# Optimization experiments

Measured on AMD Instinct MI355X. Metric: run time of the kernel, lower is better.

The kernel has to match this reference:

```python
import jax, jax.numpy as jnp
import numpy as np
from jax import lax

DIM = 256          # C
D_INNER = 512      # expand * dim
D_STATE = 16       # N
DT_RANK = 32       # ceil(d_inner / 16)
K_CONV = 4


def setup_inputs() -> dict:
    key = jax.random.key(0)
    ks = jax.random.split(key, 20)
    B, C, H, W = 2, DIM, 64, 64
    Di, N, R = D_INNER, D_STATE, DT_RANK
    s = 0.02
    inp = {
        "decoder_feat": jax.random.normal(ks[0], (B, C, H, W), jnp.float32),
        "encoder_feat": jax.random.normal(ks[1], (B, C, H, W), jnp.float32),
        # CrossMambaFusion params
        "dec_w": jax.random.normal(ks[2], (C, 2 * Di), jnp.float32) * s,
        "dec_b": jnp.zeros((2 * Di,), jnp.float32),
        "enc_w": jax.random.normal(ks[3], (C, Di), jnp.float32) * s,
        "enc_b": jnp.zeros((Di,), jnp.float32),
        "out_w": jax.random.normal(ks[4], (Di, C), jnp.float32) * s,
        "out_b": jnp.zeros((C,), jnp.float32),
        "ln_g": jnp.ones((C,), jnp.float32),
        "ln_b": jnp.zeros((C,), jnp.float32),
        # Mamba block params (inner dim = Di, expand=1.0)
        "in_w": jax.random.normal(ks[5], (Di, 2 * Di), jnp.float32) * s,
        "in_b": jnp.zeros((2 * Di,), jnp.float32),
        "conv_w": jax.random.normal(ks[6], (Di, 1, K_CONV), jnp.float32) * 0.1,
        "conv_b": jnp.zeros((Di,), jnp.float32),
        "x_proj_w": jax.random.normal(ks[7], (Di, R + 2 * N), jnp.float32) * s,
        "dt_w": jax.random.normal(ks[8], (R, Di), jnp.float32) * 0.1,
        "dt_b": jax.random.uniform(ks[9], (Di,), jnp.float32, -4.0, -2.0),  # small dt after softplus
        "A_log": jnp.log(jnp.tile(jnp.arange(1, N + 1, dtype=jnp.float32)[None, :], (Di, 1))),
        "D_param": jnp.ones((Di,), jnp.float32),
        "m_out_w": jax.random.normal(ks[10], (Di, Di), jnp.float32) * s,
        "m_out_b": jnp.zeros((Di,), jnp.float32),
    }
    return inp


def _mamba(x, in_w, in_b, conv_w, conv_b, x_proj_w, dt_w, dt_b, A_log, D_param, m_out_w, m_out_b):
    # x: (B, L, Di)
    Bsz, L, Di = x.shape
    N, R = D_STATE, DT_RANK
    xz = x @ in_w + in_b                      # (B, L, 2*Di)
    xm, z = jnp.split(xz, 2, axis=-1)
    # causal depthwise conv over the sequence axis
    xc = jnp.swapaxes(xm, 1, 2)               # (B, Di, L)
    xc = lax.conv_general_dilated(
        xc, conv_w, window_strides=(1,), padding=[(K_CONV - 1, 0)],
        dimension_numbers=("NCH", "OIH", "NCH"), feature_group_count=Di)
    xc = xc + conv_b[None, :, None]
    u = jax.nn.silu(jnp.swapaxes(xc, 1, 2))   # (B, L, Di)
    x_dbl = u @ x_proj_w                      # (B, L, R+2N)
    dt = jax.nn.softplus(x_dbl[..., :R] @ dt_w + dt_b)   # (B, L, Di)
    Bm = x_dbl[..., R:R + N]                  # (B, L, N)
    Cm = x_dbl[..., R + N:]                   # (B, L, N)
    A = -jnp.exp(A_log)                       # (Di, N)

    def step(h, t):
        dt_t, u_t, B_t, C_t = t               # (B,Di),(B,Di),(B,N),(B,N)
        dA = jnp.exp(dt_t[..., None] * A)     # (B, Di, N)
        h = h * dA + (dt_t * u_t)[..., None] * B_t[:, None, :]
        y = jnp.einsum("bdn,bn->bd", h, C_t)
        return h, y

    h0 = jnp.zeros((Bsz, Di, N), x.dtype)
    _, ys = lax.scan(step, h0, (jnp.swapaxes(dt, 0, 1), jnp.swapaxes(u, 0, 1),
                                jnp.swapaxes(Bm, 0, 1), jnp.swapaxes(Cm, 0, 1)))
    y = jnp.swapaxes(ys, 0, 1) + u * D_param  # skip connection via D
    y = y * jax.nn.silu(z)
    return y @ m_out_w + m_out_b


def reference(decoder_feat, encoder_feat, dec_w, dec_b, enc_w, enc_b, out_w, out_b,
              ln_g, ln_b, in_w, in_b, conv_w, conv_b, x_proj_w, dt_w, dt_b,
              A_log, D_param, m_out_w, m_out_b):
    B, C, H, W = decoder_feat.shape
    Di = D_INNER
    dec = jnp.transpose(decoder_feat, (0, 2, 3, 1)).reshape(B, H * W, C)
    enc = jnp.transpose(encoder_feat, (0, 2, 3, 1)).reshape(B, H * W, C)
    dec_proj = dec @ dec_w + dec_b
    dec_x, dec_gate = dec_proj[..., :Di], dec_proj[..., Di:]
    enc_p = enc @ enc_w + enc_b
    combined = dec_x * jax.nn.sigmoid(enc_p) + enc_p          # (B, L, Di)
    processed = _mamba(combined, in_w, in_b, conv_w, conv_b, x_proj_w,
                       dt_w, dt_b, A_log, D_param, m_out_w, m_out_b)
    out = (processed * jax.nn.sigmoid(dec_gate)) @ out_w + out_b
    res = out + dec
    mu = jnp.mean(res, axis=-1, keepdims=True)
    var = jnp.mean(jnp.square(res - mu), axis=-1, keepdims=True)
    res = (res - mu) * lax.rsqrt(var + 1e-5) * ln_g + ln_b
    return jnp.transpose(res.reshape(B, H, W, C), (0, 3, 1, 2))
```

## Files before the change

kernel.cpp:

```cpp
#include <hip/hip_runtime.h>
#include <hip/hip_bf16.h>

typedef __bf16 bf16x8_t __attribute__((ext_vector_type(8)));
typedef float f32x4_t __attribute__((ext_vector_type(4)));

__device__ __forceinline__ float sigmoidf_(float x) { return 1.0f / (1.0f + __expf(-x)); }
__device__ __forceinline__ float siluf_(float x) { return x * sigmoidf_(x); }
__device__ __forceinline__ float softplusf_(float x) {
    return fmaxf(x, 0.0f) + log1pf(__expf(-fabsf(x)));
}
__device__ __forceinline__ float b2f(ushort u) { return __uint_as_float(((unsigned)u) << 16); }

__global__ __launch_bounds__(256) void k_prep(
    const float* __restrict__ dec_w, const float* __restrict__ enc_w,
    const float* __restrict__ in_w, const float* __restrict__ m_out_w,
    const float* __restrict__ out_w, const float* __restrict__ x_proj_w,
    const float* __restrict__ dt_w,
    const float* __restrict__ dec, const float* __restrict__ enc,
    __hip_bfloat16* __restrict__ dec_wT, __hip_bfloat16* __restrict__ enc_wT,
    __hip_bfloat16* __restrict__ in_wT, __hip_bfloat16* __restrict__ m_out_wT,
    __hip_bfloat16* __restrict__ out_wT, __hip_bfloat16* __restrict__ xpwT,
    __hip_bfloat16* __restrict__ dtwT,
    __hip_bfloat16* __restrict__ decL, __hip_bfloat16* __restrict__ encL)
{
    __shared__ float tile[64][65];
    if (blockIdx.x < 5312) {
        int gid = blockIdx.x * 256 + threadIdx.x;
        const float* src; __hip_bfloat16* dst; int lk, N, idx;
        if (gid < 262144)       { src = dec_w;    dst = dec_wT;   lk = 8; N = 1024; idx = gid; }
        else if (gid < 393216)  { src = enc_w;    dst = enc_wT;   lk = 8; N = 512;  idx = gid - 262144; }
        else if (gid < 917504)  { src = in_w;     dst = in_wT;    lk = 9; N = 1024; idx = gid - 393216; }
        else if (gid < 1179648) { src = m_out_w;  dst = m_out_wT; lk = 9; N = 512;  idx = gid - 917504; }
        else if (gid < 1310720) { src = out_w;    dst = out_wT;   lk = 9; N = 256;  idx = gid - 1179648; }
        else if (gid < 1343488) { src = x_proj_w; dst = xpwT;     lk = 9; N = 64;   idx = gid - 1310720; }
        else                    { src = dt_w;     dst = dtwT;     lk = 5; N = 512;  idx = gid - 1343488; }
        int K = 1 << lk;
        int n = idx >> lk, k = idx & (K - 1);
        dst[idx] = __float2bfloat16(src[(size_t)k * N + n]);
        return;
    }
    const int bid = blockIdx.x - 5312;
    const int t = threadIdx.x;
    const int ct = bid & 3;
    const int lt = (bid >> 2) & 63;
    const int sel = bid >> 8;
    const int b = sel & 1, ten = sel >> 1;
    const float* src = ten ? enc : dec;
    __hip_bfloat16* dst = ten ? encL : decL;
    const size_t ibase = (size_t)b * 256 * 4096 + (size_t)(ct * 64) * 4096 + (size_t)lt * 64;
#pragma unroll
    for (int i = 0; i < 16; ++i) {
        int c = i * 4 + (t >> 6), l = t & 63;
        tile[c][l] = src[ibase + (size_t)c * 4096 + l];
    }
    __syncthreads();
    const size_t obase = ((size_t)b * 4096 + (size_t)lt * 64) * 256 + ct * 64;
#pragma unroll
    for (int i = 0; i < 16; ++i) {
        int l = i * 4 + (t >> 6), c = t & 63;
        dst[obase + (size_t)l * 256 + c] = __float2bfloat16(tile[c][l]);
    }
}

template <int EPI, int K>
__global__ __launch_bounds__(256) void bgemm(
    const __hip_bfloat16* __restrict__ A, const __hip_bfloat16* __restrict__ Bt,
    const float* __restrict__ bias, void* __restrict__ out0,
    void* __restrict__ out1, const void* __restrict__ extra)
{
    __shared__ ushort At[128 * 32];
    __shared__ ushort Bl[128 * 32];
    const int tid = threadIdx.x;
    const int wave = tid >> 6, lane = tid & 63;
    const int n0 = blockIdx.x * 128, m0 = blockIdx.y * 128;
    const int wm = (wave >> 1) * 64, wn = (wave & 1) * 64;
    f32x4_t acc[4][4] = {};
    const int fr = lane & 15, fq = (lane >> 4) * 8;

    for (int k0 = 0; k0 < K; k0 += 32) {
#pragma unroll
        for (int q = 0; q < 2; ++q) {
            int idx = q * 256 + tid;
            int row = idx >> 2, ch = (idx & 3) * 8;
            uint4 va = *(const uint4*)&A[(size_t)(m0 + row) * K + k0 + ch];
            uint4 vb = *(const uint4*)&Bt[(size_t)(n0 + row) * K + k0 + ch];
            *(uint4*)&At[row * 32 + ch] = va;
            *(uint4*)&Bl[row * 32 + ch] = vb;
        }
        __syncthreads();
        bf16x8_t af[4], bf[4];
#pragma unroll
        for (int i = 0; i < 4; ++i) {
            af[i] = *(bf16x8_t*)&At[(wm + i * 16 + fr) * 32 + fq];
            bf[i] = *(bf16x8_t*)&Bl[(wn + i * 16 + fr) * 32 + fq];
        }
#pragma unroll
        for (int i = 0; i < 4; ++i)
#pragma unroll
            for (int j = 0; j < 4; ++j)
                acc[i][j] = __builtin_amdgcn_mfma_f32_16x16x32_bf16(af[i], bf[j], acc[i][j], 0, 0, 0);
        __syncthreads();
    }

    const int col = lane & 15, rbase = (lane >> 4) * 4;
#pragma unroll
    for (int i = 0; i < 4; ++i) {
#pragma unroll
        for (int j = 0; j < 4; ++j) {
#pragma unroll
            for (int r = 0; r < 4; ++r) {
                int m = m0 + wm + i * 16 + rbase + r;
                int n = n0 + wn + j * 16 + col;
                float v = acc[i][j][r] + bias[n];
                if (EPI == 0) {
                    ((__hip_bfloat16*)out0)[(size_t)m * 512 + n] = __float2bfloat16(v);
                } else if (EPI == 1) {
                    if (n < 512) {
                        float ep = __bfloat162float(((const __hip_bfloat16*)extra)[(size_t)m * 512 + n]);
                        ((__hip_bfloat16*)out0)[(size_t)m * 512 + n] =
                            __float2bfloat16(fmaf(v, sigmoidf_(ep), ep));
                    } else {
                        ((__hip_bfloat16*)out1)[(size_t)m * 512 + (n - 512)] =
                            __float2bfloat16(sigmoidf_(v));
                    }
                } else if (EPI == 2) {
                    if (n < 512)
                        ((__hip_bfloat16*)out0)[(size_t)m * 512 + n] = __float2bfloat16(v);
                    else
                        ((__hip_bfloat16*)out1)[(size_t)m * 512 + (n - 512)] =
                            __float2bfloat16(siluf_(v));
                } else {
                    float g = __bfloat162float(((const __hip_bfloat16*)extra)[(size_t)m * 512 + n]);
                    ((__hip_bfloat16*)out0)[(size_t)m * 512 + n] = __float2bfloat16(v * g);
                }
            }
        }
    }
}

#define CROWS 16
__global__ __launch_bounds__(256) void k_conv_proj(
    const __hip_bfloat16* __restrict__ xm, const float* __restrict__ conv_w,
    const float* __restrict__ conv_b, const __hip_bfloat16* __restrict__ xpwT,
    const __hip_bfloat16* __restrict__ dtwT, const float* __restrict__ dt_b,
    __hip_bfloat16* __restrict__ u_out, float* __restrict__ Bm,
    float* __restrict__ Cm, float* __restrict__ dt_out)
{
    __shared__ ushort ut[CROWS][512 + 8];
    __shared__ ushort adt[CROWS][32 + 8];
    const int tid = threadIdx.x;
    const int wave = tid >> 6, lane = tid & 63;
    const int bl0 = blockIdx.x * CROWS;
    const int l0 = bl0 & 4095;
    const int fr = lane & 15, fq = (lane >> 4) * 8;
    const int col = lane & 15, rbase = (lane >> 4) * 4;

    {
        const int d0 = tid * 2;
        float cw0[4], cw1[4];
#pragma unroll
        for (int k = 0; k < 4; ++k) {
            cw0[k] = conv_w[d0 * 4 + k];
            cw1[k] = conv_w[d0 * 4 + 4 + k];
        }
        const float cb0 = conv_b[d0], cb1 = conv_b[d0 + 1];
        float xa[CROWS + 3], xb[CROWS + 3];
        const ushort* xs = (const ushort*)xm;
#pragma unroll
        for (int i = 0; i < CROWS + 3; ++i) {
            if (l0 - 3 + i >= 0) {
                ushort2 v = *(const ushort2*)&xs[(size_t)(bl0 - 3 + i) * 512 + d0];
                xa[i] = b2f(v.x); xb[i] = b2f(v.y);
            } else { xa[i] = 0.f; xb[i] = 0.f; }
        }
#pragma unroll
        for (int r = 0; r < CROWS; ++r) {
            float a = cb0, b = cb1;
#pragma unroll
            for (int k = 0; k < 4; ++k) {
                a = fmaf(cw0[k], xa[r + k], a);
                b = fmaf(cw1[k], xb[r + k], b);
            }
            float ua = siluf_(a), ub = siluf_(b);
            ushort2 up = make_ushort2(
                (ushort)(__bfloat16_as_ushort(__float2bfloat16(ua))),
                (ushort)(__bfloat16_as_ushort(__float2bfloat16(ub))));
            *(ushort2*)&ut[r][d0] = up;
            *(ushort2*)&((ushort*)u_out)[(size_t)(bl0 + r) * 512 + d0] = up;
        }
    }
    __syncthreads();

    {
        f32x4_t acc = {};
        const __hip_bfloat16* bp = xpwT + (size_t)(wave * 16 + fr) * 512;
#pragma unroll
        for (int k0 = 0; k0 < 512; k0 += 32) {
            bf16x8_t af = *(bf16x8_t*)&ut[fr][k0 + fq];
            bf16x8_t bf = *(const bf16x8_t*)&bp[k0 + fq];
            acc = __builtin_amdgcn_mfma_f32_16x16x32_bf16(af, bf, acc, 0, 0, 0);
        }
#pragma unroll
        for (int r = 0; r < 4; ++r) {
            int m = rbase + r;
            int n = wave * 16 + col;
            float v = acc[r];
            if (n < 32)      adt[m][n] = (ushort)__bfloat16_as_ushort(__float2bfloat16(v));
            else if (n < 48) Bm[(size_t)(bl0 + m) * 16 + (n - 32)] = v;
            else             Cm[(size_t)(bl0 + m) * 16 + (n - 48)] = v;
        }
    }
    __syncthreads();

    {
        bf16x8_t af = *(bf16x8_t*)&adt[fr][fq];
#pragma unroll
        for (int t = 0; t < 8; ++t) {
            int nt = wave * 8 + t;
            bf16x8_t bf = *(const bf16x8_t*)&dtwT[(size_t)(nt * 16 + fr) * 32 + fq];
            f32x4_t acc = {};
            acc = __builtin_amdgcn_mfma_f32_16x16x32_bf16(af, bf, acc, 0, 0, 0);
#pragma unroll
            for (int r = 0; r < 4; ++r) {
                int m = rbase + r;
                int n = nt * 16 + col;
                dt_out[(size_t)(bl0 + m) * 512 + n] = softplusf_(acc[r] + dt_b[n]);
            }
        }
    }
}

#define CHUNK 32
#define NCHUNK 128

__global__ __launch_bounds__(512) void k_scan_part(
    const float* __restrict__ dt, const __hip_bfloat16* __restrict__ u,
    const float* __restrict__ Bmp, const float* __restrict__ A_log,
    float* __restrict__ hpart, float* __restrict__ dtsums)
{
    __shared__ float Bs[CHUNK * 16];
    const int d = threadIdx.x;
    const int chunk = blockIdx.x & (NCHUNK - 1);
    const int b = blockIdx.x >> 7;
    const size_t row0 = (size_t)b * 4096 + (size_t)chunk * CHUNK;

    Bs[d] = Bmp[row0 * 16 + d];
    float Av[16];
#pragma unroll
    for (int n = 0; n < 16; n += 4) {
        float4 al = *(const float4*)&A_log[d * 16 + n];
        Av[n + 0] = -__expf(al.x);
        Av[n + 1] = -__expf(al.y);
        Av[n + 2] = -__expf(al.z);
        Av[n + 3] = -__expf(al.w);
    }
    __syncthreads();

    const float* dtp = dt + row0 * 512 + d;
    const __hip_bfloat16* up = u + row0 * 512 + d;
    float h[16] = {};
    float dtsum = 0.f;
    for (int t = 0; t < CHUNK; ++t) {
        float dtv = dtp[(size_t)t * 512];
        float uv = __bfloat162float(up[(size_t)t * 512]);
        float dtu = dtv * uv;
        dtsum += dtv;
        const float* Bt = &Bs[t * 16];
#pragma unroll
        for (int n = 0; n < 16; ++n)
            h[n] = fmaf(h[n], __expf(dtv * Av[n]), dtu * Bt[n]);
    }
    const size_t sidx = ((size_t)b * NCHUNK + chunk) * 512 + d;
    const size_t idx = sidx * 16;
#pragma unroll
    for (int n = 0; n < 16; n += 4)
        *(float4*)&hpart[idx + n] = make_float4(h[n], h[n + 1], h[n + 2], h[n + 3]);
    dtsums[sidx] = dtsum;
}

__global__ __launch_bounds__(256) void k_scan_comb(
    const float* __restrict__ hpart, const float* __restrict__ dtsums,
    const float* __restrict__ A_log, float* __restrict__ h_in)
{
    const int gid = blockIdx.x * 256 + threadIdx.x;
    const int n = gid & 15;
    const int d = (gid >> 4) & 511;
    const int b = gid >> 13;
    const float Av = -__expf(A_log[d * 16 + n]);
    float h = 0.f;
    for (int c = 0; c < NCHUNK; ++c) {
        const size_t sidx = ((size_t)b * NCHUNK + c) * 512 + d;
        const size_t idx = sidx * 16 + n;
        h_in[idx] = h;
        h = fmaf(h, __expf(Av * dtsums[sidx]), hpart[idx]);
    }
}

__global__ __launch_bounds__(512) void k_scan_fin(
    const float* __restrict__ dt, const __hip_bfloat16* __restrict__ u,
    const float* __restrict__ Bmp, const float* __restrict__ Cmp,
    const float* __restrict__ A_log, const float* __restrict__ Dp,
    const __hip_bfloat16* __restrict__ zs, const float* __restrict__ h_in,
    __hip_bfloat16* __restrict__ yout)
{
    __shared__ float Bs[CHUNK * 16];
    __shared__ float Cs[CHUNK * 16];
    const int d = threadIdx.x;
    const int chunk = blockIdx.x & (NCHUNK - 1);
    const int b = blockIdx.x >> 7;
    const size_t row0 = (size_t)b * 4096 + (size_t)chunk * CHUNK;

    Bs[d] = Bmp[row0 * 16 + d];
    Cs[d] = Cmp[row0 * 16 + d];
    float Av[16];
#pragma unroll
    for (int n = 0; n < 16; n += 4) {
        float4 al = *(const float4*)&A_log[d * 16 + n];
        Av[n + 0] = -__expf(al.x);
        Av[n + 1] = -__expf(al.y);
        Av[n + 2] = -__expf(al.z);
        Av[n + 3] = -__expf(al.w);
    }
    const float Dv = Dp[d];
    float h[16];
    const size_t idx = (((size_t)b * NCHUNK + chunk) * 512 + d) * 16;
#pragma unroll
    for (int n = 0; n < 16; n += 4) {
        float4 hv = *(const float4*)&h_in[idx + n];
        h[n] = hv.x; h[n + 1] = hv.y; h[n + 2] = hv.z; h[n + 3] = hv.w;
    }
    __syncthreads();

    const float* dtp = dt + row0 * 512 + d;
    const __hip_bfloat16* up = u + row0 * 512 + d;
    const __hip_bfloat16* zp = zs + row0 * 512 + d;
    __hip_bfloat16* yp = yout + row0 * 512 + d;
    for (int t = 0; t < CHUNK; ++t) {
        float dtv = dtp[(size_t)t * 512];
        float uv = __bfloat162float(up[(size_t)t * 512]);
        float zv = __bfloat162float(zp[(size_t)t * 512]);
        float dtu = dtv * uv;
        const float* Bt = &Bs[t * 16];
        const float* Ct = &Cs[t * 16];
        float y = 0.f;
#pragma unroll
        for (int n = 0; n < 16; ++n) {
            h[n] = fmaf(h[n], __expf(dtv * Av[n]), dtu * Bt[n]);
            y = fmaf(h[n], Ct[n], y);
        }
        yp[(size_t)t * 512] = __float2bfloat16((y + uv * Dv) * zv);
    }
}

__global__ __launch_bounds__(256) void k_out_ln(
    const __hip_bfloat16* __restrict__ A, const __hip_bfloat16* __restrict__ Bt,
    const float* __restrict__ bias, const __hip_bfloat16* __restrict__ decL,
    const float* __restrict__ ln_g, const float* __restrict__ ln_b,
    float* __restrict__ outp)
{
    __shared__ ushort At[64 * 32];
    __shared__ ushort Bl[256 * 32];
    __shared__ float red[4][64][2];
    __shared__ float lmu[64], lsc[64];
    const int tid = threadIdx.x;
    const int wave = tid >> 6, lane = tid & 63;
    const int m0 = blockIdx.x * 64;
    const int wn = wave * 64;
    f32x4_t acc[4][4] = {};
    const int fr = lane & 15, fq = (lane >> 4) * 8;

    for (int k0 = 0; k0 < 512; k0 += 32) {
        {
            int row = tid >> 2, ch = (tid & 3) * 8;
            *(uint4*)&At[row * 32 + ch] = *(const uint4*)&A[(size_t)(m0 + row) * 512 + k0 + ch];
        }
#pragma unroll
        for (int q = 0; q < 4; ++q) {
            int idx = q * 256 + tid;
            int row = idx >> 2, ch = (idx & 3) * 8;
            *(uint4*)&Bl[row * 32 + ch] = *(const uint4*)&Bt[(size_t)row * 512 + k0 + ch];
        }
        __syncthreads();
        bf16x8_t af[4], bf[4];
#pragma unroll
        for (int i = 0; i < 4; ++i) {
            af[i] = *(bf16x8_t*)&At[(i * 16 + fr) * 32 + fq];
            bf[i] = *(bf16x8_t*)&Bl[(wn + i * 16 + fr) * 32 + fq];
        }
#pragma unroll
        for (int i = 0; i < 4; ++i)
#pragma unroll
            for (int j = 0; j < 4; ++j)
                acc[i][j] = __builtin_amdgcn_mfma_f32_16x16x32_bf16(af[i], bf[j], acc[i][j], 0, 0, 0);
        __syncthreads();
    }

    const int col = lane & 15, rbase = (lane >> 4) * 4;
#pragma unroll
    for (int i = 0; i < 4; ++i) {
#pragma unroll
        for (int r = 0; r < 4; ++r) {
            int ml = i * 16 + rbase + r;
            int m = m0 + ml;
            float s = 0.f, sq = 0.f;
#pragma unroll
            for (int j = 0; j < 4; ++j) {
                int n = wn + j * 16 + col;
                float dv = b2f(((const ushort*)decL)[(size_t)m * 256 + n]);
                float v = acc[i][j][r] + bias[n] + dv;
                acc[i][j][r] = v;
                s += v;
                sq = fmaf(v, v, sq);
            }
            s += __shfl_xor(s, 1);  sq += __shfl_xor(sq, 1);
            s += __shfl_xor(s, 2);  sq += __shfl_xor(sq, 2);
            s += __shfl_xor(s, 4);  sq += __shfl_xor(sq, 4);
            s += __shfl_xor(s, 8);  sq += __shfl_xor(sq, 8);
            if (col == 0) { red[wave][ml][0] = s; red[wave][ml][1] = sq; }
        }
    }
    __syncthreads();
    if (tid < 64) {
        float s  = red[0][tid][0] + red[1][tid][0] + red[2][tid][0] + red[3][tid][0];
        float sq = red[0][tid][1] + red[1][tid][1] + red[2][tid][1] + red[3][tid][1];
        float mu = s * (1.0f / 256.0f);
        float var = sq * (1.0f / 256.0f) - mu * mu;
        lmu[tid] = mu;
        lsc[tid] = rsqrtf(var + 1e-5f);
    }
    __syncthreads();
    const int bb = m0 >> 12;
    const int lpos0 = m0 & 4095;
#pragma unroll
    for (int i = 0; i < 4; ++i) {
#pragma unroll
        for (int r = 0; r < 4; ++r) {
            int ml = i * 16 + rbase + r;
            float mu = lmu[ml], sc = lsc[ml];
#pragma unroll
            for (int j = 0; j < 4; ++j) {
                int n = wn + j * 16 + col;
                float v = (acc[i][j][r] - mu) * sc * ln_g[n] + ln_b[n];
                outp[(size_t)bb * (256 * 4096) + (size_t)n * 4096 + lpos0 + ml] = v;
            }
        }
    }
}

extern "C" void kernel_launch(void* const* d_in, const int* in_sizes, int n_in,
                              void* d_out, int out_size, void* d_ws, size_t ws_size,
                              hipStream_t stream)
{
    const float* decoder_feat = (const float*)d_in[0];
    const float* encoder_feat = (const float*)d_in[1];
    const float* dec_w = (const float*)d_in[2];
    const float* dec_b = (const float*)d_in[3];
    const float* enc_w = (const float*)d_in[4];
    const float* enc_b = (const float*)d_in[5];
    const float* out_w = (const float*)d_in[6];
    const float* out_b = (const float*)d_in[7];
    const float* ln_g = (const float*)d_in[8];
    const float* ln_bb = (const float*)d_in[9];
    const float* in_w = (const float*)d_in[10];
    const float* in_b = (const float*)d_in[11];
    const float* conv_w = (const float*)d_in[12];
    const float* conv_b = (const float*)d_in[13];
    const float* x_proj_w = (const float*)d_in[14];
    const float* dt_w = (const float*)d_in[15];
    const float* dt_b = (const float*)d_in[16];
    const float* A_log = (const float*)d_in[17];
    const float* D_param = (const float*)d_in[18];
    const float* m_out_w = (const float*)d_in[19];
    const float* m_out_b = (const float*)d_in[20];

    float* outp = (float*)d_out;
    char* ws = (char*)d_ws;
    const size_t MB = 1024ull * 1024;
    __hip_bfloat16* decL     = (__hip_bfloat16*)(ws + 0 * MB);
    __hip_bfloat16* encL     = (__hip_bfloat16*)(ws + 4 * MB);
    __hip_bfloat16* dec_wT   = (__hip_bfloat16*)(ws + 8 * MB);
    __hip_bfloat16* enc_wT   = (__hip_bfloat16*)(ws + 9 * MB);
    __hip_bfloat16* in_wT    = (__hip_bfloat16*)(ws + 10 * MB);
    __hip_bfloat16* m_out_wT = (__hip_bfloat16*)(ws + 11 * MB);
    __hip_bfloat16* out_wT   = (__hip_bfloat16*)(ws + 12 * MB);
    __hip_bfloat16* xpwT     = (__hip_bfloat16*)(ws + 12 * MB + 262144);
    __hip_bfloat16* dtwT     = (__hip_bfloat16*)(ws + 12 * MB + 262144 + 65536);
    __hip_bfloat16* enc_pb   = (__hip_bfloat16*)(ws + 13 * MB);
    __hip_bfloat16* combined = (__hip_bfloat16*)(ws + 29 * MB);
    __hip_bfloat16* gate_sig = (__hip_bfloat16*)(ws + 37 * MB);
    __hip_bfloat16* xm       = (__hip_bfloat16*)(ws + 53 * MB);
    __hip_bfloat16* z_silu   = (__hip_bfloat16*)(ws + 61 * MB);
    __hip_bfloat16* u_buf    = (__hip_bfloat16*)(ws + 69 * MB);
    float* dt_buf            = (float*)(ws + 77 * MB);
    float* Bm                = (float*)(ws + 93 * MB);
    float* Cm                = (float*)(ws + 93 * MB + 524288);
    float* hpart  = (float*)(ws + 13 * MB);
    float* dtsums = (float*)(ws + 21 * MB);
    float* h_in   = (float*)xm;
    __hip_bfloat16* y_buf = combined;
    __hip_bfloat16* gated = xm;

    k_prep<<<6336, 256, 0, stream>>>(
        dec_w, enc_w, in_w, m_out_w, out_w, x_proj_w, dt_w,
        decoder_feat, encoder_feat,
        dec_wT, enc_wT, in_wT, m_out_wT, out_wT, xpwT, dtwT, decL, encL);
    bgemm<0, 256><<<dim3(4, 64), 256, 0, stream>>>(
        encL, enc_wT, enc_b, enc_pb, nullptr, nullptr);
    bgemm<1, 256><<<dim3(8, 64), 256, 0, stream>>>(
        decL, dec_wT, dec_b, combined, gate_sig, enc_pb);
    bgemm<2, 512><<<dim3(8, 64), 256, 0, stream>>>(
        combined, in_wT, in_b, xm, z_silu, nullptr);
    k_conv_proj<<<512, 256, 0, stream>>>(
        xm, conv_w, conv_b, xpwT, dtwT, dt_b, u_buf, Bm, Cm, dt_buf);
    k_scan_part<<<2 * NCHUNK, 512, 0, stream>>>(dt_buf, u_buf, Bm, A_log, hpart, dtsums);
    k_scan_comb<<<64, 256, 0, stream>>>(hpart, dtsums, A_log, h_in);
    k_scan_fin<<<2 * NCHUNK, 512, 0, stream>>>(
        dt_buf, u_buf, Bm, Cm, A_log, D_param, z_silu, h_in, y_buf);
    bgemm<3, 512><<<dim3(4, 64), 256, 0, stream>>>(
        y_buf, m_out_wT, m_out_b, gated, nullptr, gate_sig);
    k_out_ln<<<128, 256, 0, stream>>>(
        gated, out_wT, out_b, decL, ln_g, ln_bb, outp);
}
```

Baseline: 289.2 us.

## Fuse conv/x_proj/dt projection with chunk-partial scan and store dt in bf16

Merges the conv+projection kernel and the first scan pass into one kernel per 32-row chunk. u, dt and B are kept in registers and shared memory for the partial scan instead of being reread from global memory, which removes one launch and its memory traffic. dt is now stored as bf16 rather than fp32, halving that buffer's traffic in the final scan. This costs dt precision and lowers occupancy in the fused kernel because of the larger register and shared-memory footprint (uarr[32], about 35 KB of LDS).

```diff
diff --git a/kernel.cpp b/kernel.cpp
--- a/kernel.cpp
+++ b/kernel.cpp
@@ -10,6 +10,9 @@
     return fmaxf(x, 0.0f) + log1pf(__expf(-fabsf(x)));
 }
 __device__ __forceinline__ float b2f(ushort u) { return __uint_as_float(((unsigned)u) << 16); }
+__device__ __forceinline__ ushort f2b(float f) {
+    return (ushort)__bfloat16_as_ushort(__float2bfloat16(f));
+}
 
 __global__ __launch_bounds__(256) void k_prep(
     const float* __restrict__ dec_w, const float* __restrict__ enc_w,
@@ -138,144 +141,138 @@
     }
 }
 
-#define CROWS 16
-__global__ __launch_bounds__(256) void k_conv_proj(
+#define CHUNK 32
+#define NCHUNK 128
+
+__global__ __launch_bounds__(512) void k_conv_scan(
     const __hip_bfloat16* __restrict__ xm, const float* __restrict__ conv_w,
     const float* __restrict__ conv_b, const __hip_bfloat16* __restrict__ xpwT,
     const __hip_bfloat16* __restrict__ dtwT, const float* __restrict__ dt_b,
+    const float* __restrict__ A_log,
     __hip_bfloat16* __restrict__ u_out, float* __restrict__ Bm,
-    float* __restrict__ Cm, float* __restrict__ dt_out)
-{
-    __shared__ ushort ut[CROWS][512 + 8];
-    __shared__ ushort adt[CROWS][32 + 8];
+    float* __restrict__ Cm, __hip_bfloat16* __restrict__ dt_out,
+    float* __restrict__ hpart, float* __restrict__ dtsums)
+{
+    __shared__ __align__(16) ushort us_dts[CHUNK][512 + 8];
+    __shared__ __align__(16) ushort adt[CHUNK][32 + 8];
+    __shared__ float BsL[CHUNK * 16];
+    __shared__ float CsL[CHUNK * 16];
     const int tid = threadIdx.x;
     const int wave = tid >> 6, lane = tid & 63;
-    const int bl0 = blockIdx.x * CROWS;
+    const int bl0 = blockIdx.x * CHUNK;
     const int l0 = bl0 & 4095;
+    const int b = blockIdx.x >> 7;
+    const int chunk = blockIdx.x & (NCHUNK - 1);
     const int fr = lane & 15, fq = (lane >> 4) * 8;
     const int col = lane & 15, rbase = (lane >> 4) * 4;
 
+    float uarr[CHUNK];
     {
-        const int d0 = tid * 2;
-        float cw0[4], cw1[4];
-#pragma unroll
-        for (int k = 0; k < 4; ++k) {
-            cw0[k] = conv_w[d0 * 4 + k];
-            cw1[k] = conv_w[d0 * 4 + 4 + k];
-        }
-        const float cb0 = conv_b[d0], cb1 = conv_b[d0 + 1];
-        float xa[CROWS + 3], xb[CROWS + 3];
+        const int d = tid;
+        const float cw0 = conv_w[d * 4], cw1 = conv_w[d * 4 + 1];
+        const float cw2 = conv_w[d * 4 + 2], cw3 = conv_w[d * 4 + 3];
+        const float cb = conv_b[d];
         const ushort* xs = (const ushort*)xm;
-#pragma unroll
-        for (int i = 0; i < CROWS + 3; ++i) {
-            if (l0 - 3 + i >= 0) {
-                ushort2 v = *(const ushort2*)&xs[(size_t)(bl0 - 3 + i) * 512 + d0];
-                xa[i] = b2f(v.x); xb[i] = b2f(v.y);
-            } else { xa[i] = 0.f; xb[i] = 0.f; }
-        }
-#pragma unroll
-        for (int r = 0; r < CROWS; ++r) {
-            float a = cb0, b = cb1;
-#pragma unroll
-            for (int k = 0; k < 4; ++k) {
-                a = fmaf(cw0[k], xa[r + k], a);
-                b = fmaf(cw1[k], xb[r + k], b);
-            }
-            float ua = siluf_(a), ub = siluf_(b);
-            ushort2 up = make_ushort2(
-                (ushort)(__bfloat16_as_ushort(__float2bfloat16(ua))),
-                (ushort)(__bfloat16_as_ushort(__float2bfloat16(ub))));
-            *(ushort2*)&ut[r][d0] = up;
-            *(ushort2*)&((ushort*)u_out)[(size_t)(bl0 + r) * 512 + d0] = up;
+        float x0 = (l0 >= 3) ? b2f(xs[(size_t)(bl0 - 3) * 512 + d]) : 0.f;
+        float x1 = (l0 >= 2) ? b2f(xs[(size_t)(bl0 - 2) * 512 + d]) : 0.f;
+        float x2 = (l0 >= 1) ? b2f(xs[(size_t)(bl0 - 1) * 512 + d]) : 0.f;
+#pragma unroll
+        for (int t = 0; t < CHUNK; ++t) {
+            float x3 = b2f(xs[(size_t)(bl0 + t) * 512 + d]);
+            float a = cb;
+            a = fmaf(cw0, x0, a);
+            a = fmaf(cw1, x1, a);
+            a = fmaf(cw2, x2, a);
+            a = fmaf(cw3, x3, a);
+            float uv = siluf_(a);
+            uarr[t] = uv;
+            ushort ub = f2b(uv);
+            us_dts[t][d] = ub;
+            ((ushort*)u_out)[(size_t)(bl0 + t) * 512 + d] = ub;
+            x0 = x1; x1 = x2; x2 = x3;
         }
     }
     __syncthreads();
 
     {
+        const int mi = wave >> 2, n0w = (wave & 3) * 16;
         f32x4_t acc = {};
-        const __hip_bfloat16* bp = xpwT + (size_t)(wave * 16 + fr) * 512;
+        const __hip_bfloat16* bp = xpwT + (size_t)(n0w + fr) * 512;
 #pragma unroll
         for (int k0 = 0; k0 < 512; k0 += 32) {
-            bf16x8_t af = *(bf16x8_t*)&ut[fr][k0 + fq];
+            bf16x8_t af = *(bf16x8_t*)&us_dts[mi * 16 + fr][k0 + fq];
             bf16x8_t bf = *(const bf16x8_t*)&bp[k0 + fq];
             acc = __builtin_amdgcn_mfma_f32_16x16x32_bf16(af, bf, acc, 0, 0, 0);
         }
 #pragma unroll
         for (int r = 0; r < 4; ++r) {
-            int m = rbase + r;
-            int n = wave * 16 + col;
+            int m = mi * 16 + rbase + r;
+            int n = n0w + col;
             float v = acc[r];
-            if (n < 32)      adt[m][n] = (ushort)__bfloat16_as_ushort(__float2bfloat16(v));
-            else if (n < 48) Bm[(size_t)(bl0 + m) * 16 + (n - 32)] = v;
-            else             Cm[(size_t)(bl0 + m) * 16 + (n - 48)] = v;
+            if (n < 32) {
+                adt[m][n] = f2b(v);
+            } else if (n < 48) {
+                BsL[m * 16 + (n - 32)] = v;
+                Bm[(size_t)(bl0 + m) * 16 + (n - 32)] = v;
+            } else {
+                CsL[m * 16 + (n - 48)] = v;
+                Cm[(size_t)(bl0 + m) * 16 + (n - 48)] = v;
+            }
         }
     }
     __syncthreads();
 
     {
-        bf16x8_t af = *(bf16x8_t*)&adt[fr][fq];
+        const int mi = wave >> 2;
+        bf16x8_t af = *(bf16x8_t*)&adt[mi * 16 + fr][fq];
 #pragma unroll
         for (int t = 0; t < 8; ++t) {
-            int nt = wave * 8 + t;
+            int nt = (wave & 3) * 8 + t;
             bf16x8_t bf = *(const bf16x8_t*)&dtwT[(size_t)(nt * 16 + fr) * 32 + fq];
             f32x4_t acc = {};
             acc = __builtin_amdgcn_mfma_f32_16x16x32_bf16(af, bf, acc, 0, 0, 0);
 #pragma unroll
             for (int r = 0; r < 4; ++r) {
-                int m = rbase + r;
+                int m = mi * 16 + rbase + r;
                 int n = nt * 16 + col;
-                dt_out[(size_t)(bl0 + m) * 512 + n] = softplusf_(acc[r] + dt_b[n]);
+                ushort dv = f2b(softplusf_(acc[r] + dt_b[n]));
+                us_dts[m][n] = dv;
+                ((ushort*)dt_out)[(size_t)(bl0 + m) * 512 + n] = dv;
             }
         }
     }
-}
-
-#define CHUNK 32
-#define NCHUNK 128
-
-__global__ __launch_bounds__(512) void k_scan_part(
-    const float* __restrict__ dt, const __hip_bfloat16* __restrict__ u,
-    const float* __restrict__ Bmp, const float* __restrict__ A_log,
-    float* __restrict__ hpart, float* __restrict__ dtsums)
-{
-    __shared__ float Bs[CHUNK * 16];
-    const int d = threadIdx.x;
-    const int chunk = blockIdx.x & (NCHUNK - 1);
-    const int b = blockIdx.x >> 7;
-    const size_t row0 = (size_t)b * 4096 + (size_t)chunk * CHUNK;
-
-    Bs[d] = Bmp[row0 * 16 + d];
-    float Av[16];
-#pragma unroll
-    for (int n = 0; n < 16; n += 4) {
-        float4 al = *(const float4*)&A_log[d * 16 + n];
-        Av[n + 0] = -__expf(al.x);
-        Av[n + 1] = -__expf(al.y);
-        Av[n + 2] = -__expf(al.z);
-        Av[n + 3] = -__expf(al.w);
-    }
-    __syncthreads();
-
-    const float* dtp = dt + row0 * 512 + d;
-    const __hip_bfloat16* up = u + row0 * 512 + d;
-    float h[16] = {};
-    float dtsum = 0.f;
-    for (int t = 0; t < CHUNK; ++t) {
-        float dtv = dtp[(size_t)t * 512];
-        float uv = __bfloat162float(up[(size_t)t * 512]);
-        float dtu = dtv * uv;
-        dtsum += dtv;
-        const float* Bt = &Bs[t * 16];
-#pragma unroll
-        for (int n = 0; n < 16; ++n)
-            h[n] = fmaf(h[n], __expf(dtv * Av[n]), dtu * Bt[n]);
-    }
-    const size_t sidx = ((size_t)b * NCHUNK + chunk) * 512 + d;
-    const size_t idx = sidx * 16;
-#pragma unroll
-    for (int n = 0; n < 16; n += 4)
-        *(float4*)&hpart[idx + n] = make_float4(h[n], h[n + 1], h[n + 2], h[n + 3]);
-    dtsums[sidx] = dtsum;
+    __syncthreads();
+
+    {
+        const int d = tid;
+        float Av[16];
+#pragma unroll
+        for (int n = 0; n < 16; n += 4) {
+            float4 al = *(const float4*)&A_log[d * 16 + n];
+            Av[n + 0] = -__expf(al.x);
+            Av[n + 1] = -__expf(al.y);
+            Av[n + 2] = -__expf(al.z);
+            Av[n + 3] = -__expf(al.w);
+        }
+        float h[16] = {};
+        float dtsum = 0.f;
+#pragma unroll
+        for (int t = 0; t < CHUNK; ++t) {
+            float dtv = b2f(us_dts[t][d]);
+            float dtu = dtv * uarr[t];
+            dtsum += dtv;
+            const float* Bt = &BsL[t * 16];
+#pragma unroll
+            for (int n = 0; n < 16; ++n)
+                h[n] = fmaf(h[n], __expf(dtv * Av[n]), dtu * Bt[n]);
+        }
+        const size_t sidx = ((size_t)b * NCHUNK + chunk) * 512 + d;
+        const size_t idx = sidx * 16;
+#pragma unroll
+        for (int n = 0; n < 16; n += 4)
+            *(float4*)&hpart[idx + n] = make_float4(h[n], h[n + 1], h[n + 2], h[n + 3]);
+        dtsums[sidx] = dtsum;
+    }
 }
 
 __global__ __launch_bounds__(256) void k_scan_comb(
@@ -297,7 +294,7 @@
 }
 
 __global__ __launch_bounds__(512) void k_scan_fin(
-    const float* __restrict__ dt, const __hip_bfloat16* __restrict__ u,
+    const __hip_bfloat16* __restrict__ dt, const __hip_bfloat16* __restrict__ u,
     const float* __restrict__ Bmp, const float* __restrict__ Cmp,
     const float* __restrict__ A_log, const float* __restrict__ Dp,
     const __hip_bfloat16* __restrict__ zs, const float* __restrict__ h_in,
@@ -331,14 +328,14 @@
     }
     __syncthreads();
 
-    const float* dtp = dt + row0 * 512 + d;
-    const __hip_bfloat16* up = u + row0 * 512 + d;
-    const __hip_bfloat16* zp = zs + row0 * 512 + d;
+    const ushort* dtp = (const ushort*)dt + row0 * 512 + d;
+    const ushort* up = (const ushort*)u + row0 * 512 + d;
+    const ushort* zp = (const ushort*)zs + row0 * 512 + d;
     __hip_bfloat16* yp = yout + row0 * 512 + d;
     for (int t = 0; t < CHUNK; ++t) {
-        float dtv = dtp[(size_t)t * 512];
-        float uv = __bfloat162float(up[(size_t)t * 512]);
-        float zv = __bfloat162float(zp[(size_t)t * 512]);
+        float dtv = b2f(dtp[(size_t)t * 512]);
+        float uv = b2f(up[(size_t)t * 512]);
+        float zv = b2f(zp[(size_t)t * 512]);
         float dtu = dtv * uv;
         const float* Bt = &Bs[t * 16];
         const float* Ct = &Cs[t * 16];
@@ -491,7 +488,7 @@
     __hip_bfloat16* xm       = (__hip_bfloat16*)(ws + 53 * MB);
     __hip_bfloat16* z_silu   = (__hip_bfloat16*)(ws + 61 * MB);
     __hip_bfloat16* u_buf    = (__hip_bfloat16*)(ws + 69 * MB);
-    float* dt_buf            = (float*)(ws + 77 * MB);
+    __hip_bfloat16* dt_buf   = (__hip_bfloat16*)(ws + 77 * MB);
     float* Bm                = (float*)(ws + 93 * MB);
     float* Cm                = (float*)(ws + 93 * MB + 524288);
     float* hpart  = (float*)(ws + 13 * MB);
@@ -510,9 +507,9 @@
         decL, dec_wT, dec_b, combined, gate_sig, enc_pb);
     bgemm<2, 512><<<dim3(8, 64), 256, 0, stream>>>(
         combined, in_wT, in_b, xm, z_silu, nullptr);
-    k_conv_proj<<<512, 256, 0, stream>>>(
-        xm, conv_w, conv_b, xpwT, dtwT, dt_b, u_buf, Bm, Cm, dt_buf);
-    k_scan_part<<<2 * NCHUNK, 512, 0, stream>>>(dt_buf, u_buf, Bm, A_log, hpart, dtsums);
+    k_conv_scan<<<2 * NCHUNK, 512, 0, stream>>>(
+        xm, conv_w, conv_b, xpwT, dtwT, dt_b, A_log,
+        u_buf, Bm, Cm, dt_buf, hpart, dtsums);
     k_scan_comb<<<64, 256, 0, stream>>>(hpart, dtsums, A_log, h_in);
     k_scan_fin<<<2 * NCHUNK, 512, 0, stream>>>(
         dt_buf, u_buf, Bm, Cm, A_log, D_param, z_silu, h_in, y_buf);
```

Result: no change. 284.7 us (-1.6%).
